# Kernel optimization log

Hardware: AMD Instinct MI355X
Metric: run time of the kernel (lower is better)

## Reference

```python
import jax, jax.numpy as jnp
import numpy as np

EPS = float(np.finfo(float).eps)
NUM_RFS = 1

def conv3d(x, w):
    # x: [N,C,D,H,W], w: [O,I,kd,kh,kw], VALID, stride 1 (matches F.conv3d defaults)
    return jax.lax.conv_general_dilated(
        x, w, window_strides=(1, 1, 1), padding='VALID',
        dimension_numbers=('NCDHW', 'OIDHW', 'NCDHW'))

def setup_inputs() -> dict:
    key = jax.random.key(0)
    k1, k2, k3, k4 = jax.random.split(key, 4)
    x = jax.random.normal(k1, (1, 1, 3, 394, 394), jnp.float32)
    x_prev = jax.random.normal(k2, (1, 1, 3, 394, 394), jnp.float32)
    # params stored post-permute as [out_ch, in_ch, kt, kh, kw]
    filts_temp = jax.random.normal(k3, (16, 1, 3, 11, 11), jnp.float32)
    filts_notemp = jax.random.normal(k4, (16, 1, 1, 11, 11), jnp.float32)
    return {"x": x, "x_prev": x_prev, "filts_temp": filts_temp, "filts_notemp": filts_notemp}

def reference(x, x_prev, filts_temp, filts_notemp):
    corr_x = NUM_RFS * filts_temp.shape[3]  # kh
    corr_y = NUM_RFS * filts_temp.shape[4]  # kw
    num_filts = filts_temp.shape[0] + filts_notemp.shape[0]

    def feats(v):
        vt = jax.nn.relu(conv3d(v, filts_temp)) / 2           # [1,16,1,H',W'] (T==kt)
        vn = jax.nn.relu(conv3d(v[:, :, -1:, :, :], filts_notemp))  # last frame, [1,16,1,H',W']
        return jnp.concatenate([vt, vn], axis=1)              # [1,32,1,H',W']

    f = feats(x)
    fp = feats(x_prev)
    # channel-wise normalization
    x1 = f / (jnp.sum(f, axis=1, keepdims=True) + EPS)
    x1_prev = fp / (jnp.sum(fp, axis=1, keepdims=True) + EPS)

    y_max, x_max = x1.shape[3], x1.shape[4]
    yc = y_max - 2 * corr_y
    xc = x_max - 2 * corr_x
    # cropped current-frame channels become conv filters: [nf,1,1,yc,xc]
    x1_filts = x1[:, :, :, corr_y:y_max - corr_y, corr_x:x_max - corr_x].reshape(
        num_filts, 1, 1, yc, xc)
    prev = x1_prev.reshape(1, 1, num_filts, y_max, x_max)
    # normalized cross-correlation via conv3d: out [1, nf, nf, 2cy+1, 2cx+1]
    x2 = conv3d(prev, x1_filts)
    x2 = x2.reshape(1, num_filts, num_filts, 2 * corr_y + 1, 2 * corr_x + 1)
    x2 = x2 / ((y_max - 2 * corr_y) * (x_max - 2 * corr_y))  # faithful to original (uses corr_y twice)
    return x1, x2
```

## Files before the change

kernel.cpp:

```cpp
#include <hip/hip_runtime.h>
#include <hip/hip_bf16.h>


typedef unsigned short ushort_t;
typedef unsigned int uint_t;
typedef unsigned char uchar_t;
typedef __attribute__((ext_vector_type(4))) float f32x4;
typedef __attribute__((ext_vector_type(16))) float f32x16;
typedef __attribute__((ext_vector_type(4))) uint_t uint4_t;
typedef __attribute__((ext_vector_type(2))) uint_t uint2_t;

#define EPSF 2.2204460492503131e-16f
#define X1_N (32*384*384)
#define X2_N (32*32*23*23)

#define FILTB_ROW_B 12288
#define FILTB_BYTES (372*48*32*8)
#define PREVB_STRIDE 432
#define PREVB_BYTES (32*385*PREVB_STRIDE)
#define ZERO_BYTES ((size_t)FILTB_BYTES + PREVB_BYTES)
#define FT2_ELEMS (16*45*12)

#define YMAX 367
#define NCHUNKS 16
#define INV_AREA (1.0f/131044.0f)

#define SB_COPY_B 432
#define SB_DYB_B  (8*SB_COPY_B)
#define SB_ROW_B  (4*SB_DYB_B)
#define SB_BYTES  (2*2*SB_ROW_B)

#define SA_BYTES  (8*FILTB_ROW_B)
#define SMEM_TOTAL (SA_BYTES + SB_BYTES)

__device__ __forceinline__ uint_t f32_to_e4m3(float f) {
  if (f < 0.015625f)
    return (uint_t)__float2int_rn(f * 512.0f);
  uint_t b = __builtin_bit_cast(uint_t, f);
  int e = (int)(b >> 23) - 127;
  uint_t m = b & 0x7FFFFFu;
  uint_t keep = m >> 20;
  uint_t rest = m & 0xFFFFFu;
  keep += (rest > 0x80000u) || (rest == 0x80000u && (keep & 1u));
  if (keep == 8u) { keep = 0u; e += 1; }
  if (e > 8) return 0x7Eu;
  return (uint_t)(((e + 7) << 3) | keep);
}

__global__ void prep_kernel(const float* __restrict__ ft, const float* __restrict__ fn,
                            float* __restrict__ fT2)
{
  const int e = blockIdx.x * 256 + threadIdx.x;
  if (e < FT2_ELEMS) {
    const int chp = e / 540;
    const int rem = e - chp * 540;
    const int row = rem / 12;
    const int j = rem - row * 12;
    float v = 0.f;
    if (j < 11) {
      if (row < 33)      v = ft[chp * 363 + row * 11 + j];
      else if (row < 44) v = fn[chp * 121 + (row - 33) * 11 + j];
    }
    fT2[e] = v;
  }
}

__global__ __launch_bounds__(128, 4) void feat_kernel(
    const float* __restrict__ xcur, const float* __restrict__ xprev,
    const float* __restrict__ fT2,
    float* __restrict__ out_x1, uchar_t* __restrict__ prevb)
{
  __shared__ float sPx[3 * 18 * 28];
  const int tid = threadIdx.x;
  const int chp = tid & 15;
  const int r = tid >> 4;
  const int j0 = blockIdx.x * 16;
  const int i0 = blockIdx.y * 8;
  const int i = i0 + r;
  const int mode = blockIdx.z;
  const float* __restrict__ xin = mode ? xprev : xcur;

  for (int e = tid; e < 3 * 18 * 26; e += 128) {
    const int t = e / 468;
    const int rem = e - t * 468;
    const int ri = rem / 26;
    const int ci = rem - ri * 26;
    sPx[(t * 18 + ri) * 28 + ci] = xin[((size_t)t * 394 + i0 + ri) * 394 + j0 + ci];
  }
  __syncthreads();

  const float* __restrict__ fbase = fT2 + chp * 540;

  float accT[16], accN[16];
#pragma unroll
  for (int p = 0; p < 16; ++p) { accT[p] = 0.f; accN[p] = 0.f; }

#pragma unroll
  for (int t = 0; t < 3; ++t) {
    for (int a = 0; a < 11; ++a) {
      const float* row = &sPx[(t * 18 + r + a) * 28];
      float wv[26];
#pragma unroll
      for (int k = 0; k < 6; ++k) {
        const f32x4 q = *(const f32x4*)(row + 4 * k);
        wv[4 * k + 0] = q[0]; wv[4 * k + 1] = q[1];
        wv[4 * k + 2] = q[2]; wv[4 * k + 3] = q[3];
      }
      wv[24] = row[24]; wv[25] = row[25];

      const float* fr = fbase + (t * 11 + a) * 12;
      const f32x4 fq0 = *(const f32x4*)(fr);
      const f32x4 fq1 = *(const f32x4*)(fr + 4);
      const f32x4 fq2 = *(const f32x4*)(fr + 8);
      float fv[12];
#pragma unroll
      for (int k = 0; k < 4; ++k) { fv[k] = fq0[k]; fv[4+k] = fq1[k]; fv[8+k] = fq2[k]; }
      float fv2[12];
      if (t == 2) {
        const float* fr2 = fbase + (33 + a) * 12;
        const f32x4 g0 = *(const f32x4*)(fr2);
        const f32x4 g1 = *(const f32x4*)(fr2 + 4);
        const f32x4 g2 = *(const f32x4*)(fr2 + 8);
#pragma unroll
        for (int k = 0; k < 4; ++k) { fv2[k] = g0[k]; fv2[4+k] = g1[k]; fv2[8+k] = g2[k]; }
      }

#pragma unroll
      for (int b = 0; b < 11; ++b) {
        const float fT = fv[b];
#pragma unroll
        for (int p = 0; p < 16; ++p) accT[p] = fmaf(wv[b + p], fT, accT[p]);
        if (t == 2) {
          const float fN = fv2[b];
#pragma unroll
          for (int p = 0; p < 16; ++p) accN[p] = fmaf(wv[b + p], fN, accN[p]);
        }
      }
    }
  }

  float o0[16], o1[16];
#pragma unroll
  for (int p = 0; p < 16; ++p) {
    const float vT = fmaxf(accT[p], 0.f) * 0.5f;
    const float vN = fmaxf(accN[p], 0.f);
    float s = vT + vN;
    s += __shfl_xor(s, 1);  s += __shfl_xor(s, 2);
    s += __shfl_xor(s, 4);  s += __shfl_xor(s, 8);
    const float inv = 1.f / (s + EPSF);
    o0[p] = vT * inv;
    o1[p] = vN * inv;
  }

  if (mode == 0) {
#pragma unroll
    for (int q = 0; q < 4; ++q) {
      f32x4 v0 = {o0[4*q], o0[4*q+1], o0[4*q+2], o0[4*q+3]};
      f32x4 v1 = {o1[4*q], o1[4*q+1], o1[4*q+2], o1[4*q+3]};
      *(f32x4*)(out_x1 + (size_t)chp * 147456 + i * 384 + j0 + 4 * q) = v0;
      *(f32x4*)(out_x1 + (size_t)(chp + 16) * 147456 + i * 384 + j0 + 4 * q) = v1;
    }
  } else {
    uint4_t u0, u1;
#pragma unroll
    for (int q = 0; q < 4; ++q) {
      u0[q] = f32_to_e4m3(o0[4*q]) | (f32_to_e4m3(o0[4*q+1]) << 8) |
              (f32_to_e4m3(o0[4*q+2]) << 16) | (f32_to_e4m3(o0[4*q+3]) << 24);
      u1[q] = f32_to_e4m3(o1[4*q]) | (f32_to_e4m3(o1[4*q+1]) << 8) |
              (f32_to_e4m3(o1[4*q+2]) << 16) | (f32_to_e4m3(o1[4*q+3]) << 24);
    }
    *(uint4_t*)(prevb + ((size_t)chp * 385 + i) * PREVB_STRIDE + j0) = u0;
    *(uint4_t*)(prevb + ((size_t)(chp + 16) * 385 + i) * PREVB_STRIDE + j0) = u1;
  }
}

__global__ __launch_bounds__(256) void pack_kernel(
    const float* __restrict__ x1, uchar_t* __restrict__ filtb)
{
  const int e = blockIdx.x * 256 + threadIdx.x;
  if (e >= 362 * 46 * 32) return;
  const int o = e & 31;
  const int q = e >> 5;
  const int xb = q % 46;
  const int rowr = q / 46 + 5;
  const int i = rowr + 6;
  const int j0 = 11 + xb * 8;
  const float* src = x1 + (size_t)o * 147456 + i * 384 + j0;
  uint_t w0 = 0, w1 = 0;
#pragma unroll
  for (int k = 0; k < 4; ++k) {
    w0 |= f32_to_e4m3((j0 + k     <= 372) ? src[k]     : 0.f) << (8 * k);
    w1 |= f32_to_e4m3((j0 + 4 + k <= 372) ? src[4 + k] : 0.f) << (8 * k);
  }
  uint2_t u = {w0, w1};
  *(uint2_t*)(filtb + (((size_t)(rowr * 48 + xb) * 32 + o) << 3)) = u;
}

__global__ __launch_bounds__(768, 3) void corr_kernel(
    const uchar_t* __restrict__ filtb, const uchar_t* __restrict__ prevb,
    float* __restrict__ x2)
{
  extern __shared__ uchar_t smem[];

  const int tid = threadIdx.x;
  const int lane = tid & 63;
  const int wv = tid >> 6;
  const int cg = (wv >= 6) ? 1 : 0;
  const int w = wv - 6 * cg;
  const int kg = lane >> 5;
  const int nn = lane & 31;

  const int chpair = blockIdx.x / NCHUNKS;
  const int chunk = blockIdx.x % NCHUNKS;
  const int ch = 2 * chpair + cg;
  const int y0 = (chunk * YMAX) / NCHUNKS;
  const int y1 = ((chunk + 1) * YMAX) / NCHUNKS;

  uint_t* const sBg = (uint_t*)(smem + SA_BYTES) + cg * (2 * (SB_ROW_B / 4));

  int boffB[3];
#pragma unroll
  for (int nt = 0; nt < 3; ++nt) {
    const int n = nt * 32 + nn;
    const int dyb = n / 24;
    const int dxr = n - 24 * dyb;
    const int dx = (dxr < 23) ? dxr : 22;
    const int s = dx & 7;
    boffB[nt] = dyb * SB_DYB_B + s * SB_COPY_B + (dx >> 3) * 8 + kg * 8;
  }

  const int tl = tid - cg * 384;
  const bool st_act = (tl < 104);
  const int sdyb = st_act ? (tl / 26) : 0;
  const int sg = tl - 26 * (st_act ? (tl / 26) : 0);
  const uchar_t* srcbase = prevb + ((size_t)(ch * 385 + 6 * sdyb)) * PREVB_STRIDE;
  const int dstoff = sdyb * (SB_DYB_B / 4) + 4 * sg;

  uint_t st0 = 0, st1 = 0, st2 = 0, st3 = 0, st4 = 0, st5 = 0;

  auto load_st = [&](int yy) {
    const uint_t* sw = (const uint_t*)(srcbase + (size_t)yy * PREVB_STRIDE) + 4 * sg;
    const uint4_t lo = *(const uint4_t*)(sw);
    const uint2_t hi = *(const uint2_t*)(sw + 4);
    st0 = lo.x; st1 = lo.y; st2 = lo.z; st3 = lo.w; st4 = hi.x; st5 = hi.y;
  };

  auto write_shift = [&](int buf) {
    uint_t* dst = sBg + buf * (SB_ROW_B / 4) + dstoff;
    const uint_t wd[6] = {st0, st1, st2, st3, st4, st5};
#pragma unroll
    for (int s = 0; s < 8; ++s) {
      const int off = s >> 2;
      const int b = (s & 3) * 8;
      uint4_t v;
      if (b == 0) {
        v = uint4_t{wd[off], wd[off + 1], wd[off + 2], wd[off + 3]};
      } else {
        v = uint4_t{(wd[off]     >> b) | (wd[off + 1] << (32 - b)),
                    (wd[off + 1] >> b) | (wd[off + 2] << (32 - b)),
                    (wd[off + 2] >> b) | (wd[off + 3] << (32 - b)),
                    (wd[off + 3] >> b) | (wd[off + 4] << (32 - b))};
      }
      *(uint4_t*)(dst + s * (SB_COPY_B / 4)) = v;
    }
  };

  f32x16 acc[3];
#pragma unroll
  for (int nt = 0; nt < 3; ++nt)
#pragma unroll
    for (int r = 0; r < 16; ++r) acc[nt][r] = 0.f;

  {
    uint4_t pv[6];
#pragma unroll
    for (int r6 = 0; r6 < 6; ++r6)
      pv[r6] = *(const uint4_t*)(filtb + (size_t)(y0 + r6) * FILTB_ROW_B + tid * 16);
#pragma unroll
    for (int r6 = 0; r6 < 6; ++r6)
      *(uint4_t*)(smem + ((y0 + r6) & 7) * FILTB_ROW_B + tid * 16) = pv[r6];
  }
  if (st_act) {
    load_st(y0);
    write_shift(0);
    if (y0 + 1 < y1) load_st(y0 + 1);
  }

  __syncthreads();

  for (int y = y0; y < y1; ++y) {
    const int pb = (y - y0) & 1;

    const bool a_act = (y + 6 <= y1 + 4);
    uint4_t aval;
    if (a_act)
      aval = *(const uint4_t*)(filtb + (size_t)(y + 6) * FILTB_ROW_B + tid * 16);

    if (st_act && y + 1 < y1) write_shift(pb ^ 1);
    if (st_act && y + 2 < y1) load_st(y + 2);

    const char* sBrd = (const char*)sBg + pb * SB_ROW_B;
    const char* aRow = (const char*)smem +
        ((y + 5 - w) & 7) * FILTB_ROW_B + kg * 256 + nn * 8;

    long Af, Afn, Bf[3], Bfn[3];
    Af = *(const long*)(aRow);
#pragma unroll
    for (int nt = 0; nt < 3; ++nt)
      Bf[nt] = *(const long*)(sBrd + boffB[nt]);

#pragma unroll
    for (int Kt = 0; Kt < 24; ++Kt) {
      const int Ktn = (Kt + 1 < 24) ? Kt + 1 : 23;
      Afn = *(const long*)(aRow + (Ktn << 9));
#pragma unroll
      for (int nt = 0; nt < 3; ++nt)
        Bfn[nt] = *(const long*)(sBrd + boffB[nt] + (Ktn << 4));
#pragma unroll
      for (int nt = 0; nt < 3; ++nt)
        acc[nt] = __builtin_amdgcn_mfma_f32_32x32x16_fp8_fp8(
            Af, Bf[nt], acc[nt], 0, 0, 0);
      Af = Afn;
#pragma unroll
      for (int nt = 0; nt < 3; ++nt) Bf[nt] = Bfn[nt];
    }

    if (a_act)
      *(uint4_t*)(smem + ((y + 6) & 7) * FILTB_ROW_B + tid * 16) = aval;

    __syncthreads();
  }

#pragma unroll
  for (int nt = 0; nt < 3; ++nt) {
    const int n = nt * 32 + nn;
    const int dyb = n / 24;
    const int dxr = n - 24 * dyb;
    if (dxr < 23) {
      const int dy = w + 6 * dyb;
      if (dy <= 22) {
#pragma unroll
        for (int r = 0; r < 16; ++r) {
          const int o = (r & 3) + 8 * (r >> 2) + 4 * kg;
          atomicAdd(&x2[((o * 32 + ch) * 23 + dy) * 23 + dxr],
                    acc[nt][r] * INV_AREA);
        }
      }
    }
  }
}

extern "C" void kernel_launch(void* const* d_in, const int* in_sizes, int n_in,
                              void* d_out, int out_size, void* d_ws, size_t ws_size,
                              hipStream_t stream)
{
  const float* x     = (const float*)d_in[0];
  const float* xprev = (const float*)d_in[1];
  const float* ft    = (const float*)d_in[2];
  const float* fn    = (const float*)d_in[3];
  float* out = (float*)d_out;

  uchar_t* filtb = (uchar_t*)d_ws;
  uchar_t* prevb = filtb + FILTB_BYTES;
  float* fT2 = (float*)(prevb + PREVB_BYTES);

  static bool attr_set = false;
  if (!attr_set) {
    (void)hipFuncSetAttribute((const void*)corr_kernel,
        hipFuncAttributeMaxDynamicSharedMemorySize, SMEM_TOTAL);
    attr_set = true;
  }

  hipMemsetAsync(d_ws, 0, ZERO_BYTES, stream);
  hipMemsetAsync(out + X1_N, 0, (size_t)X2_N * sizeof(float), stream);

  prep_kernel<<<dim3((FT2_ELEMS + 255) / 256), 256, 0, stream>>>(ft, fn, fT2);
  feat_kernel<<<dim3(24, 48, 2), 128, 0, stream>>>(x, xprev, fT2, out, prevb);
  pack_kernel<<<dim3((362 * 46 * 32 + 255) / 256), 256, 0, stream>>>(out, filtb);
  corr_kernel<<<dim3(16 * NCHUNKS), 768, SMEM_TOTAL, stream>>>(
      filtb, prevb, out + X1_N);
}
```

Baseline: 293.7 us.

## Switch correlation MFMA to 32x32x64 scaled fp8 with matching filter layout

Replaces the 32x32x16 fp8 MFMA inner loop (24 k-steps) with the gfx950 scaled 32x32x64 f8f6f4 MFMA (6 k-steps), using unit scales. The filter-packing kernel writes a new interleaved byte layout so each lane can fetch 32 contiguous K bytes with two 16-byte LDS reads, and the B offsets are adjusted to match. The aim is fewer MFMA issues and wider LDS loads per step. The cost is more registers per operand, and correctness depends on the new K ordering lining up between A and B.

```diff
diff --git a/kernel.cpp b/kernel.cpp
--- a/kernel.cpp
+++ b/kernel.cpp
@@ -9,6 +9,7 @@
 typedef __attribute__((ext_vector_type(16))) float f32x16;
 typedef __attribute__((ext_vector_type(4))) uint_t uint4_t;
 typedef __attribute__((ext_vector_type(2))) uint_t uint2_t;
+typedef __attribute__((ext_vector_type(8))) int int8v;
 
 #define EPSF 2.2204460492503131e-16f
 #define X1_N (32*384*384)
@@ -193,7 +194,9 @@
     w1 |= f32_to_e4m3((j0 + 4 + k <= 372) ? src[4 + k] : 0.f) << (8 * k);
   }
   uint2_t u = {w0, w1};
-  *(uint2_t*)(filtb + (((size_t)(rowr * 48 + xb) * 32 + o) << 3)) = u;
+  const int off = (xb >> 3) * 2048 + ((xb >> 1) & 1) * 1024 +
+                  ((xb >> 2) & 1) * 512 + o * 16 + (xb & 1) * 8;
+  *(uint2_t*)(filtb + (size_t)rowr * FILTB_ROW_B + off) = u;
 }
 
 __global__ __launch_bounds__(768, 3) void corr_kernel(
@@ -226,7 +229,7 @@
     const int dxr = n - 24 * dyb;
     const int dx = (dxr < 23) ? dxr : 22;
     const int s = dx & 7;
-    boffB[nt] = dyb * SB_DYB_B + s * SB_COPY_B + (dx >> 3) * 8 + kg * 8;
+    boffB[nt] = dyb * SB_DYB_B + s * SB_COPY_B + (dx >> 3) * 8 + kg * 32;
   }
 
   const int tl = tid - cg * 384;
@@ -265,6 +268,23 @@
     }
   };
 
+  auto loadA = [](const char* aRow, int kt) -> int8v {
+    const uint4_t a0 = *(const uint4_t*)(aRow + kt * 2048);
+    const uint4_t a1 = *(const uint4_t*)(aRow + kt * 2048 + 1024);
+    int8v r = {(int)a0.x, (int)a0.y, (int)a0.z, (int)a0.w,
+               (int)a1.x, (int)a1.y, (int)a1.z, (int)a1.w};
+    return r;
+  };
+  auto loadB = [](const char* p) -> int8v {
+    const uint2_t b0 = *(const uint2_t*)(p);
+    const uint2_t b1 = *(const uint2_t*)(p + 8);
+    const uint2_t b2 = *(const uint2_t*)(p + 16);
+    const uint2_t b3 = *(const uint2_t*)(p + 24);
+    int8v r = {(int)b0.x, (int)b0.y, (int)b1.x, (int)b1.y,
+               (int)b2.x, (int)b2.y, (int)b3.x, (int)b3.y};
+    return r;
+  };
+
   f32x16 acc[3];
 #pragma unroll
   for (int nt = 0; nt < 3; ++nt)
@@ -301,25 +321,26 @@
 
     const char* sBrd = (const char*)sBg + pb * SB_ROW_B;
     const char* aRow = (const char*)smem +
-        ((y + 5 - w) & 7) * FILTB_ROW_B + kg * 256 + nn * 8;
-
-    long Af, Afn, Bf[3], Bfn[3];
-    Af = *(const long*)(aRow);
+        ((y + 5 - w) & 7) * FILTB_ROW_B + kg * 512 + nn * 16;
+
+    int8v Af, Afn, Bf[3], Bfn[3];
+    Af = loadA(aRow, 0);
 #pragma unroll
     for (int nt = 0; nt < 3; ++nt)
-      Bf[nt] = *(const long*)(sBrd + boffB[nt]);
-
-#pragma unroll
-    for (int Kt = 0; Kt < 24; ++Kt) {
-      const int Ktn = (Kt + 1 < 24) ? Kt + 1 : 23;
-      Afn = *(const long*)(aRow + (Ktn << 9));
+      Bf[nt] = loadB(sBrd + boffB[nt]);
+
+#pragma unroll
+    for (int kt = 0; kt < 6; ++kt) {
+      const int ktn = (kt + 1 < 6) ? kt + 1 : 5;
+      Afn = loadA(aRow, ktn);
 #pragma unroll
       for (int nt = 0; nt < 3; ++nt)
-        Bfn[nt] = *(const long*)(sBrd + boffB[nt] + (Ktn << 4));
+        Bfn[nt] = loadB(sBrd + boffB[nt] + (ktn << 6));
 #pragma unroll
       for (int nt = 0; nt < 3; ++nt)
-        acc[nt] = __builtin_amdgcn_mfma_f32_32x32x16_fp8_fp8(
-            Af, Bf[nt], acc[nt], 0, 0, 0);
+        acc[nt] = __builtin_amdgcn_mfma_scale_f32_32x32x64_f8f6f4(
+            Af, Bf[nt], acc[nt], 0, 0,
+            0, 0x7F7F7F7F, 0, 0x7F7F7F7F);
       Af = Afn;
 #pragma unroll
       for (int nt = 0; nt < 3; ++nt) Bf[nt] = Bfn[nt];
```

After: 753.2 us. 2.56x slower.
